# Kernel optimization log

Hardware: AMD Instinct MI355X
Metric: run time of the kernel (lower is better)

The kernel has to match this reference:

```python
import jax, jax.numpy as jnp
import numpy as np

NEG_INF = -1e30  # stands in for -inf; safe under fp16/bf16 softmax too


def setup_inputs() -> dict:
    key = jax.random.key(0)
    k1, k2, k3, k4 = jax.random.split(key, 4)
    B, M, N, V, A = 16, 512, 512, 1024, 1024
    q = jax.random.normal(k1, (B, M, V), dtype=jnp.float32)
    p = jax.random.normal(k2, (B, N, V), dtype=jnp.float32)
    q_mask = jnp.ones((B, M), dtype=jnp.int32)  # 1 = real token
    p_mask = jnp.ones((B, N), dtype=jnp.int32)
    # xavier_normal: std = sqrt(2/(fan_in+fan_out))
    std = np.sqrt(2.0 / (V + A)).astype(np.float32)
    W1 = jax.random.normal(k3, (A, V), dtype=jnp.float32) * std
    W2 = jax.random.normal(k4, (A, V), dtype=jnp.float32) * std
    return {"q": q, "p": p, "q_mask": q_mask, "p_mask": p_mask, "W1": W1, "W2": W2}


def reference(q, p, q_mask, p_mask, W1, W2):
    # Projections with ReLU (bias-free linears)
    s_q = jax.nn.relu(jnp.einsum('bmv,av->bma', q, W1))  # [B,M,A]
    s_p = jax.nn.relu(jnp.einsum('bnv,av->bna', p, W2))  # [B,N,A]
    # Shared score matrix s[b,m,n]
    s = jnp.einsum('bma,bna->bmn', s_q, s_p)
    # Direction 1: attend over p (mask pad columns of p), softmax over n
    s_to_p = jnp.where(p_mask[:, None, :] == 0, NEG_INF, s)
    weights_p = jax.nn.softmax(s_to_p, axis=2)            # [B,M,N]
    output_q = jnp.einsum('bmn,bnv->bmv', weights_p, p)   # [B,M,V]
    # Direction 2: transpose, attend over q (mask pad columns of q)
    s_to_q = jnp.where(q_mask[:, None, :] == 0, NEG_INF, jnp.swapaxes(s, 1, 2))
    weights_q = jax.nn.softmax(s_to_q, axis=2)            # [B,N,M]
    output_p = jnp.einsum('bnm,bmv->bnv', weights_q, q)   # [B,N,V]
    # Dropout is identity in eval mode (training=False)
    return (output_p, output_q)
```

## Files before the change

kernel.cpp:

```cpp
#include <hip/hip_runtime.h>


#define AS1 __attribute__((address_space(1)))
#define AS3 __attribute__((address_space(3)))

typedef _Float16 f16x8 __attribute__((ext_vector_type(8)));
typedef _Float16 f16x4 __attribute__((ext_vector_type(4)));
typedef float f32x4 __attribute__((ext_vector_type(4)));

__device__ __forceinline__ long tswz(int r, int k, int ktiles) {
  return ((long)((r >> 7) * ktiles + (k >> 5)) << 12)
       + ((long)(r & 127) << 5)
       + ((((k >> 3) & 3) ^ ((r >> 1) & 3)) << 3) + (k & 7);
}

__global__ __launch_bounds__(256) void prep_all(
    const float* __restrict__ q, const float* __restrict__ p,
    const float* __restrict__ W1, const float* __restrict__ W2,
    _Float16* __restrict__ xdst, _Float16* __restrict__ wdst)
{
  long g = (long)blockIdx.x * 256 + threadIdx.x;
  int rg = (int)(g >> 7);
  int c8 = ((int)g & 127) << 3;
  const float* srow;
  _Float16* dst;
  long off;
  if (rg < 8192) {
    srow = q + (long)rg * 1024 + c8; dst = xdst; off = tswz(rg, c8, 32);
  } else if (rg < 16384) {
    srow = p + (long)(rg - 8192) * 1024 + c8; dst = xdst; off = tswz(rg, c8, 32);
  } else {
    int r2 = rg - 16384;
    srow = (r2 < 1024 ? W1 + (long)r2 * 1024 : W2 + (long)(r2 - 1024) * 1024) + c8;
    dst = wdst; off = tswz(r2, c8, 32);
  }
  const float4* s4 = (const float4*)srow;
  float4 f0 = s4[0], f1 = s4[1];
  f16x8 hh;
  hh[0]=(_Float16)f0.x; hh[1]=(_Float16)f0.y; hh[2]=(_Float16)f0.z; hh[3]=(_Float16)f0.w;
  hh[4]=(_Float16)f1.x; hh[5]=(_Float16)f1.y; hh[6]=(_Float16)f1.z; hh[7]=(_Float16)f1.w;
  *(f16x8*)(dst + off) = hh;
}

__global__ __launch_bounds__(256) void prep_xT2(
    const _Float16* __restrict__ xh, _Float16* __restrict__ dstT)
{
  __shared__ _Float16 t[64][72];
  const int x = blockIdx.x, y = blockIdx.y, zz = blockIdx.z;
  const int rbase = (zz < 16) ? (8192 + zz * 512) : ((zz - 16) * 512);
  const int tid = threadIdx.x;
  for (int it = 0; it < 2; ++it) {
    int id = it * 256 + tid;
    int mloc = id >> 3, v8 = (id & 7) << 3;
    f16x8 v = *(const f16x8*)(xh + tswz(rbase + y * 64 + mloc, x * 64 + v8, 32));
    *(f16x8*)(&t[mloc][v8]) = v;
  }
  __syncthreads();
  _Float16* db = dstT + (long)zz * 524288;
  for (int it = 0; it < 2; ++it) {
    int id = it * 256 + tid;
    int c = id >> 3, ch = id & 7;
    int v = x * 64 + c, mb = y * 64 + ch * 8;
    f16x8 hh;
#pragma unroll
    for (int i = 0; i < 8; ++i) hh[i] = t[ch * 8 + i][c];
    *(f16x8*)(db + tswz(v, mb, 16)) = hh;
  }
}

template<bool RELU, int OUTMODE>
__global__ __launch_bounds__(512, 2) void gemm256_dp(
    const _Float16* __restrict__ A, const _Float16* __restrict__ B,
    float* __restrict__ Cf, _Float16* __restrict__ Ch,
    const int ktiles, const int ldc,
    const long aBatchTiles, const long bBatchTiles, const long cBatchElems,
    const int cTilesRow, const long cOff0, const long cOff1, const int cSplit)
{
  __shared__ _Float16 sA[4][8192];
  __shared__ _Float16 sB[4][8192];

  const int gx = gridDim.x, gy = gridDim.y;
  long nwg = (long)gx * gy * gridDim.z;
  long bid = blockIdx.x + (long)gx * (blockIdx.y + (long)gy * blockIdx.z);
  long chunk = nwg >> 3;
  long o = (bid & 7) * chunk + (bid >> 3);
  const int bx = (int)(o % gx);
  const int by = (int)((o / gx) % gy);
  const int bz = (int)(o / ((long)gx * gy));

  const int tid = threadIdx.x;
  const int lane = tid & 63, w = tid >> 6;
  const int wm = w >> 2, wn = w & 3;
  const int lrow = lane & 15, kg = lane >> 4;
  const int swz = (lrow >> 1) & 3;

  const long aT0 = (long)bz * aBatchTiles + (long)(2 * by) * ktiles;
  const long bT0 = (long)bz * bBatchTiles + (long)(2 * bx) * ktiles;
  const int NKT = ktiles;

  auto stage = [&](int kt) {
    const int buf = kt & 3;
#pragma unroll
    for (int h = 0; h < 2; ++h) {
      __builtin_amdgcn_global_load_lds(
          (const AS1 void*)(A + ((aT0 + h * ktiles + kt) << 12) + w * 512 + lane * 8),
          (AS3 void*)(&sA[buf][h * 4096 + w * 512]), 16, 0, 0);
      __builtin_amdgcn_global_load_lds(
          (const AS1 void*)(B + ((bT0 + h * ktiles + kt) << 12) + w * 512 + lane * 8),
          (AS3 void*)(&sB[buf][h * 4096 + w * 512]), 16, 0, 0);
    }
  };

  const char* aF = (const char*)&sA[0][0] + wm * 8192 + lrow * 64 + ((kg ^ swz) << 4);
  const char* bF = (const char*)&sB[0][0] + (wn >> 1) * 8192
                 + ((wn & 1) * 64 + lrow) * 64 + ((kg ^ swz) << 4);

  f32x4 acc[8][4] = {};

  stage(0); stage(1); stage(2);

  for (int kt = 0; kt < NKT; ++kt) {
    if (kt < NKT - 2)       asm volatile("s_waitcnt vmcnt(8)" ::: "memory");
    else if (kt == NKT - 2) asm volatile("s_waitcnt vmcnt(4)" ::: "memory");
    else                    asm volatile("s_waitcnt vmcnt(0)" ::: "memory");
    __builtin_amdgcn_s_barrier();
    __builtin_amdgcn_sched_barrier(0);
    const int bo = (kt & 3) * 16384;
    f16x8 fa[8], fb[4];
#pragma unroll
    for (int i = 0; i < 8; ++i) fa[i] = *(const f16x8*)(aF + bo + i * 1024);
#pragma unroll
    for (int i = 0; i < 4; ++i) fb[i] = *(const f16x8*)(bF + bo + i * 1024);
    if (kt + 3 < NKT) stage(kt + 3);
    __builtin_amdgcn_s_setprio(1);
#pragma unroll
    for (int mi = 0; mi < 8; ++mi)
#pragma unroll
      for (int ni = 0; ni < 4; ++ni)
        acc[mi][ni] = __builtin_amdgcn_mfma_f32_16x16x32_f16(fb[ni], fa[mi], acc[mi][ni], 0, 0, 0);
    __builtin_amdgcn_s_setprio(0);
  }

  const int m0 = by * 256 + wm * 128 + lrow;
  const int b0 = bx * 256 + wn * 64 + (kg << 2);
  if (OUTMODE == 1) {
    long cbase = cSplit ? (bz < 16 ? cOff0 + (long)bz * cBatchElems
                                   : cOff1 + (long)(bz - 16) * cBatchElems)
                        : (long)bz * cBatchElems;
    float* Cb = Cf + cbase;
#pragma unroll
    for (int mi = 0; mi < 8; ++mi)
#pragma unroll
      for (int ni = 0; ni < 4; ++ni)
        *(f32x4*)(Cb + (long)(m0 + mi * 16) * ldc + b0 + ni * 16) = acc[mi][ni];
  } else {
    _Float16* Cb = Ch + (long)bz * cBatchElems;
#pragma unroll
    for (int mi = 0; mi < 8; ++mi)
#pragma unroll
      for (int ni = 0; ni < 4; ++ni) {
        f16x4 hv;
#pragma unroll
        for (int r2 = 0; r2 < 4; ++r2) {
          float x = acc[mi][ni][r2];
          if (RELU) x = fmaxf(x, 0.0f);
          hv[r2] = (_Float16)x;
        }
        *(f16x4*)(Cb + tswz(m0 + mi * 16, b0 + ni * 16, cTilesRow)) = hv;
      }
  }
}

__global__ __launch_bounds__(256, 2) void gemm_dp(
    const _Float16* __restrict__ Ah, const _Float16* __restrict__ B,
    float* __restrict__ Cf,
    const int ktiles, const int ldc,
    const long aBatchTiles, const long bBatchTiles, const long cBatchElems)
{
  __shared__ _Float16 sA[4][4096];
  __shared__ _Float16 sB[4][4096];

  const int gx = gridDim.x, gy = gridDim.y;
  long nwg = (long)gx * gy * gridDim.z;
  long bid = blockIdx.x + (long)gx * (blockIdx.y + (long)gy * blockIdx.z);
  long chunk = nwg >> 3;
  long o = (bid & 7) * chunk + (bid >> 3);
  const int bx = (int)(o % gx);
  const int by = (int)((o / gx) % gy);
  const int bz = (int)(o / ((long)gx * gy));

  const int tid = threadIdx.x;
  const int lane = tid & 63, w = tid >> 6;
  const int wa = w >> 1, wb = w & 1;
  const int lrow = lane & 15, kg = lane >> 4;
  const int swz = (lrow >> 1) & 3;

  const long aT0 = (long)bz * aBatchTiles + (long)by * ktiles;
  const long bT0 = (long)bz * bBatchTiles + (long)bx * ktiles;
  const int NKT = ktiles;

  auto stage = [&](int kt) {
    const int buf = kt & 3;
    const long ta = (aT0 + kt) << 12;
    const long tb = (bT0 + kt) << 12;
#pragma unroll
    for (int j = 0; j < 2; ++j) {
      __builtin_amdgcn_global_load_lds(
          (const AS1 void*)(Ah + ta + j * 2048 + w * 512 + lane * 8),
          (AS3 void*)(&sA[buf][j * 2048 + w * 512]), 16, 0, 0);
      __builtin_amdgcn_global_load_lds(
          (const AS1 void*)(B + tb + j * 2048 + w * 512 + lane * 8),
          (AS3 void*)(&sB[buf][j * 2048 + w * 512]), 16, 0, 0);
    }
  };

  const char* aF = (const char*)&sA[0][0] + (wa * 64 + lrow) * 64 + ((kg ^ swz) << 4);
  const char* bF = (const char*)&sB[0][0] + (wb * 64 + lrow) * 64 + ((kg ^ swz) << 4);

  f32x4 acc[4][4] = {};

  stage(0); stage(1); stage(2);

  for (int kt = 0; kt < NKT; ++kt) {
    if (kt < NKT - 2)       asm volatile("s_waitcnt vmcnt(8)" ::: "memory");
    else if (kt == NKT - 2) asm volatile("s_waitcnt vmcnt(4)" ::: "memory");
    else                    asm volatile("s_waitcnt vmcnt(0)" ::: "memory");
    __builtin_amdgcn_s_barrier();
    __builtin_amdgcn_sched_barrier(0);
    const int bo = (kt & 3) * 8192;
    f16x8 fa[4], fb[4];
#pragma unroll
    for (int i = 0; i < 4; ++i) fa[i] = *(const f16x8*)(aF + bo + i * 1024);
#pragma unroll
    for (int i = 0; i < 4; ++i) fb[i] = *(const f16x8*)(bF + bo + i * 1024);
    if (kt + 3 < NKT) stage(kt + 3);
    __builtin_amdgcn_s_setprio(1);
#pragma unroll
    for (int mi = 0; mi < 4; ++mi)
#pragma unroll
      for (int ni = 0; ni < 4; ++ni)
        acc[mi][ni] = __builtin_amdgcn_mfma_f32_16x16x32_f16(fb[ni], fa[mi], acc[mi][ni], 0, 0, 0);
    __builtin_amdgcn_s_setprio(0);
  }

  float* Cb = Cf + (long)bz * cBatchElems;
  const int m0 = by * 128 + wa * 64 + lrow;
  const int n0 = bx * 128 + wb * 64 + (kg << 2);
#pragma unroll
  for (int mi = 0; mi < 4; ++mi)
#pragma unroll
    for (int ni = 0; ni < 4; ++ni)
      *(f32x4*)(Cb + (long)(m0 + mi * 16) * ldc + n0 + ni * 16) = acc[mi][ni];
}

__global__ __launch_bounds__(256) void softmax_row(
    const float* __restrict__ S, const int* __restrict__ mask, _Float16* __restrict__ W)
{
  const int row = blockIdx.x, b = row >> 9, m = row & 511;
  const float* Sr = S + (long)row * 512;
  const int* mr = mask + (long)b * 512;
  const int tid = threadIdx.x;
  const int lane = tid & 63, wave = tid >> 6;
  __shared__ float red[4];

  float v0 = mr[tid] ? Sr[tid] : -1e30f;
  float v1 = mr[tid + 256] ? Sr[tid + 256] : -1e30f;
  float mx = fmaxf(v0, v1);
#pragma unroll
  for (int of = 32; of >= 1; of >>= 1) mx = fmaxf(mx, __shfl_xor(mx, of, 64));
  if (lane == 0) red[wave] = mx;
  __syncthreads();
  mx = fmaxf(fmaxf(red[0], red[1]), fmaxf(red[2], red[3]));
  __syncthreads();
  float e0 = __expf(v0 - mx), e1 = __expf(v1 - mx);
  float sm = e0 + e1;
#pragma unroll
  for (int of = 32; of >= 1; of >>= 1) sm += __shfl_xor(sm, of, 64);
  if (lane == 0) red[wave] = sm;
  __syncthreads();
  float inv = 1.0f / (red[0] + red[1] + red[2] + red[3]);

  _Float16* Wb = W + (long)b * 262144;
  Wb[tswz(m, tid, 16)] = (_Float16)(e0 * inv);
  Wb[tswz(m, tid + 256, 16)] = (_Float16)(e1 * inv);
}

__global__ __launch_bounds__(256) void softmax_col(
    const float* __restrict__ S, const int* __restrict__ mask, _Float16* __restrict__ W)
{
  __shared__ float ldsT[32][513];
  const int n0 = blockIdx.x * 32, b = blockIdx.y;
  const float* Sb = S + (long)b * 262144;
  const int* mr = mask + (long)b * 512;
  const int tid = threadIdx.x;
  const int lane = tid & 63, w = tid >> 6;

  for (int it = 0; it < 64; ++it) {
    int m = it * 8 + (tid >> 5);
    int c = tid & 31;
    float v = mr[m] ? Sb[(long)m * 512 + n0 + c] : -1e30f;
    ldsT[c][m] = v;
  }
  __syncthreads();

  _Float16* Wb = W + (long)b * 262144;
#pragma unroll
  for (int cc = 0; cc < 8; ++cc) {
    int col = w * 8 + cc;
    float v[8];
#pragma unroll
    for (int j = 0; j < 8; ++j) v[j] = ldsT[col][lane + 64 * j];
    float mx = v[0];
#pragma unroll
    for (int j = 1; j < 8; ++j) mx = fmaxf(mx, v[j]);
#pragma unroll
    for (int of = 32; of >= 1; of >>= 1) mx = fmaxf(mx, __shfl_xor(mx, of, 64));
    float e[8], sm = 0.0f;
#pragma unroll
    for (int j = 0; j < 8; ++j) { e[j] = __expf(v[j] - mx); sm += e[j]; }
#pragma unroll
    for (int of = 32; of >= 1; of >>= 1) sm += __shfl_xor(sm, of, 64);
    float inv = 1.0f / sm;
    int n = n0 + col;
#pragma unroll
    for (int j = 0; j < 8; ++j)
      Wb[tswz(n, lane + 64 * j, 16)] = (_Float16)(e[j] * inv);
  }
}

extern "C" void kernel_launch(void* const* d_in, const int* in_sizes, int n_in,
                              void* d_out, int out_size, void* d_ws, size_t ws_size,
                              hipStream_t stream) {
  const float* q = (const float*)d_in[0];
  const float* p = (const float*)d_in[1];
  const int* q_mask = (const int*)d_in[2];
  const int* p_mask = (const int*)d_in[3];
  const float* W1 = (const float*)d_in[4];
  const float* W2 = (const float*)d_in[5];
  float* out = (float*)d_out;

  char* ws = (char*)d_ws;
  const size_t MB = 1048576;
  _Float16* W1h = (_Float16*)(ws + 0 * MB);
  _Float16* qh  = (_Float16*)(ws + 4 * MB);
  _Float16* sqh = (_Float16*)(ws + 36 * MB);
  float*    s   = (float*)(ws + 68 * MB);
  _Float16* pT  = (_Float16*)(ws + 36 * MB);
  _Float16* wp  = (_Float16*)(ws + 4 * MB);
  _Float16* wq  = (_Float16*)(ws + 12 * MB);

  dim3 blk(256);

  prep_all<<<9216, blk, 0, stream>>>(q, p, W1, W2, qh, W1h);

  gemm256_dp<true, 2><<<dim3(4, 32, 2), dim3(512), 0, stream>>>(
      qh, W1h, nullptr, sqh,
      32, 0,
      2048, 256, 8388608L,
      32, 0, 0, 0);

  gemm_dp<<<dim3(4, 4, 16), blk, 0, stream>>>(
      sqh, (_Float16*)(ws + 52 * MB), s, 32, 512,
      128, 128, 262144L);

  prep_xT2<<<dim3(16, 8, 32), blk, 0, stream>>>(qh, pT);

  softmax_row<<<8192, blk, 0, stream>>>(s, p_mask, wp);
  softmax_col<<<dim3(16, 16), blk, 0, stream>>>(s, q_mask, wq);

  gemm256_dp<false, 1><<<dim3(4, 2, 32), dim3(512), 0, stream>>>(
      wp, pT, out, nullptr,
      16, 1024,
      64, 128, 524288L,
      0, 8388608L, 0L, 1);
}
```

Baseline: 151.5 us.

## Deepen score-GEMM K-stage to 64 and issue prefetch before LDS reads

The batched score GEMM now loads 64-wide K slices per stage into a triple buffer instead of 32-wide slices into a quad buffer. This halves the number of barriers and waitcnt points per K loop. In both GEMM kernels the async global-to-LDS prefetch is now issued right after the barrier, ahead of the fragment reads, so memory traffic starts earlier. The larger shared-memory footprint (about 96 KB per block) may allow fewer resident blocks per CU than the two the launch bounds request.

```diff
diff --git a/kernel.cpp b/kernel.cpp
--- a/kernel.cpp
+++ b/kernel.cpp
@@ -125,13 +125,13 @@
     else                    asm volatile("s_waitcnt vmcnt(0)" ::: "memory");
     __builtin_amdgcn_s_barrier();
     __builtin_amdgcn_sched_barrier(0);
+    if (kt + 3 < NKT) stage(kt + 3);
     const int bo = (kt & 3) * 16384;
     f16x8 fa[8], fb[4];
 #pragma unroll
     for (int i = 0; i < 8; ++i) fa[i] = *(const f16x8*)(aF + bo + i * 1024);
 #pragma unroll
     for (int i = 0; i < 4; ++i) fb[i] = *(const f16x8*)(bF + bo + i * 1024);
-    if (kt + 3 < NKT) stage(kt + 3);
     __builtin_amdgcn_s_setprio(1);
 #pragma unroll
     for (int mi = 0; mi < 8; ++mi)
@@ -171,14 +171,14 @@
   }
 }
 
-__global__ __launch_bounds__(256, 2) void gemm_dp(
+__global__ __launch_bounds__(256, 2) void gemm_dp64(
     const _Float16* __restrict__ Ah, const _Float16* __restrict__ B,
     float* __restrict__ Cf,
-    const int ktiles, const int ldc,
+    const int ktiles32, const int ldc,
     const long aBatchTiles, const long bBatchTiles, const long cBatchElems)
 {
-  __shared__ _Float16 sA[4][4096];
-  __shared__ _Float16 sB[4][4096];
+  __shared__ _Float16 sA[3][8192];
+  __shared__ _Float16 sB[3][8192];
 
   const int gx = gridDim.x, gy = gridDim.y;
   long nwg = (long)gx * gy * gridDim.z;
@@ -195,22 +195,25 @@
   const int lrow = lane & 15, kg = lane >> 4;
   const int swz = (lrow >> 1) & 3;
 
-  const long aT0 = (long)bz * aBatchTiles + (long)by * ktiles;
-  const long bT0 = (long)bz * bBatchTiles + (long)bx * ktiles;
-  const int NKT = ktiles;
+  const long aT0 = (long)bz * aBatchTiles + (long)by * ktiles32;
+  const long bT0 = (long)bz * bBatchTiles + (long)bx * ktiles32;
+  const int NKT = ktiles32 >> 1;
 
   auto stage = [&](int kt) {
-    const int buf = kt & 3;
-    const long ta = (aT0 + kt) << 12;
-    const long tb = (bT0 + kt) << 12;
+    const int buf = kt % 3;
 #pragma unroll
     for (int j = 0; j < 2; ++j) {
-      __builtin_amdgcn_global_load_lds(
-          (const AS1 void*)(Ah + ta + j * 2048 + w * 512 + lane * 8),
-          (AS3 void*)(&sA[buf][j * 2048 + w * 512]), 16, 0, 0);
-      __builtin_amdgcn_global_load_lds(
-          (const AS1 void*)(B + tb + j * 2048 + w * 512 + lane * 8),
-          (AS3 void*)(&sB[buf][j * 2048 + w * 512]), 16, 0, 0);
+      const long ta = (aT0 + 2 * kt + j) << 12;
+      const long tb = (bT0 + 2 * kt + j) << 12;
+#pragma unroll
+      for (int l = 0; l < 2; ++l) {
+        __builtin_amdgcn_global_load_lds(
+            (const AS1 void*)(Ah + ta + (l * 256 + tid) * 8),
+            (AS3 void*)(&sA[buf][j * 4096 + (l * 256 + tid) * 8]), 16, 0, 0);
+        __builtin_amdgcn_global_load_lds(
+            (const AS1 void*)(B + tb + (l * 256 + tid) * 8),
+            (AS3 void*)(&sB[buf][j * 4096 + (l * 256 + tid) * 8]), 16, 0, 0);
+      }
     }
   };
 
@@ -219,28 +222,30 @@
 
   f32x4 acc[4][4] = {};
 
-  stage(0); stage(1); stage(2);
+  stage(0); stage(1);
 
   for (int kt = 0; kt < NKT; ++kt) {
-    if (kt < NKT - 2)       asm volatile("s_waitcnt vmcnt(8)" ::: "memory");
-    else if (kt == NKT - 2) asm volatile("s_waitcnt vmcnt(4)" ::: "memory");
-    else                    asm volatile("s_waitcnt vmcnt(0)" ::: "memory");
+    if (kt < NKT - 1) asm volatile("s_waitcnt vmcnt(8)" ::: "memory");
+    else              asm volatile("s_waitcnt vmcnt(0)" ::: "memory");
     __builtin_amdgcn_s_barrier();
     __builtin_amdgcn_sched_barrier(0);
-    const int bo = (kt & 3) * 8192;
-    f16x8 fa[4], fb[4];
-#pragma unroll
-    for (int i = 0; i < 4; ++i) fa[i] = *(const f16x8*)(aF + bo + i * 1024);
-#pragma unroll
-    for (int i = 0; i < 4; ++i) fb[i] = *(const f16x8*)(bF + bo + i * 1024);
-    if (kt + 3 < NKT) stage(kt + 3);
-    __builtin_amdgcn_s_setprio(1);
-#pragma unroll
-    for (int mi = 0; mi < 4; ++mi)
-#pragma unroll
-      for (int ni = 0; ni < 4; ++ni)
-        acc[mi][ni] = __builtin_amdgcn_mfma_f32_16x16x32_f16(fb[ni], fa[mi], acc[mi][ni], 0, 0, 0);
-    __builtin_amdgcn_s_setprio(0);
+    if (kt + 2 < NKT) stage(kt + 2);
+    const int bo = (kt % 3) * 16384;
+#pragma unroll
+    for (int sub = 0; sub < 2; ++sub) {
+      f16x8 fa[4], fb[4];
+#pragma unroll
+      for (int i = 0; i < 4; ++i) fa[i] = *(const f16x8*)(aF + bo + sub * 8192 + i * 1024);
+#pragma unroll
+      for (int i = 0; i < 4; ++i) fb[i] = *(const f16x8*)(bF + bo + sub * 8192 + i * 1024);
+      __builtin_amdgcn_s_setprio(1);
+#pragma unroll
+      for (int mi = 0; mi < 4; ++mi)
+#pragma unroll
+        for (int ni = 0; ni < 4; ++ni)
+          acc[mi][ni] = __builtin_amdgcn_mfma_f32_16x16x32_f16(fb[ni], fa[mi], acc[mi][ni], 0, 0, 0);
+      __builtin_amdgcn_s_setprio(0);
+    }
   }
 
   float* Cb = Cf + (long)bz * cBatchElems;
@@ -359,7 +364,7 @@
       2048, 256, 8388608L,
       32, 0, 0, 0);
 
-  gemm_dp<<<dim3(4, 4, 16), blk, 0, stream>>>(
+  gemm_dp64<<<dim3(4, 4, 16), blk, 0, stream>>>(
       sqh, (_Float16*)(ws + 52 * MB), s, 32, 512,
       128, 128, 262144L);
 
```

Measured after the change: 167.0 us. 10.3% more time.
